# Kernel tuning notes

Measured on AMD Instinct MI355X. Metric: run time of the kernel, lower is better.

Reference implementation:

```python
import jax, jax.numpy as jnp
import numpy as np

C = 1203      # num_classes
P = 0.8       # mitigation exponent
Q = 2.0       # compensation exponent
EPS = 0.01
LOSS_WEIGHT = 1.0


def setup_inputs() -> dict:
    key = jax.random.key(0)
    k1, k2 = jax.random.split(key)
    N = 32768
    cls_score = jax.random.normal(k1, (N, C + 2), dtype=jnp.float32)
    labels = jax.random.randint(k2, (N,), 0, C, dtype=jnp.int64)  # all positive RoIs
    label_weights = jnp.ones((N,), dtype=jnp.float32)
    return {
        'cls_score': cls_score,
        'labels': labels,
        'label_weights': label_weights,
        'avg_factor': N,
    }


def _seesaw_loss(cls_score, labels, label_weights, avg_factor):
    N = cls_score.shape[0]
    rows = jnp.arange(N)

    # cum_samples buffer: starts at zero, incremented by per-class counts this step
    cum = jnp.zeros((C + 1,), cls_score.dtype).at[labels].add(1.0)

    # one-hot multi-labels over C+1 channels (last channel is background, unused since all labels < C)
    m_labels = jax.nn.one_hot(labels, C + 1, dtype=cls_score.dtype)  # [N, C+1]

    csc = cls_score[:, :C]   # class logits [N, C]
    csb = cls_score[:, C:]   # binary (pos/neg) logits [N, 2]

    # --- seesaw weights ---
    cum_c = jnp.maximum(cum, 1.0)
    ratio = cum_c[None, :] / cum_c[:, None]                 # [C+1, C+1]
    sample_w = jnp.where(ratio < 1.0, ratio ** P, 1.0)
    mitigation = sample_w[labels]                           # [N, C+1]

    scores = jax.lax.stop_gradient(jax.nn.softmax(csc, axis=1))  # detached
    self_scores = scores[rows, labels]                      # [N]
    score_mat = scores / jnp.maximum(self_scores, EPS)[:, None]  # [N, C]
    compensation = jnp.where(score_mat > 1.0, score_mat ** Q, 1.0)

    seesaw = mitigation.at[:, :C].multiply(compensation)    # [N, C+1]

    # add log seesaw weights to negative-class logits
    adj = csc + (jnp.log(seesaw) * (1.0 - m_labels))[:, :C]  # [N, C]

    # --- multi-label cross entropy (per-row masked logsumexp + softplus) ---
    lw = label_weights[:, None]
    pos_mask = m_labels[:, :C] * lw            # [N, C]
    neg_mask = (1.0 - m_labels[:, :C]) * lw
    ninf = jnp.array(-jnp.inf, adj.dtype)
    pos_lse = jax.nn.logsumexp(jnp.where(pos_mask == 1.0, -adj, ninf), axis=1)
    neg_lse = jax.nn.logsumexp(jnp.where(neg_mask == 1.0, adj, ninf), axis=1)
    inv_pos_log = -jnp.log(pos_mask.sum(axis=1))
    loss_classes = LOSS_WEIGHT * jax.nn.softplus(inv_pos_log + pos_lse + neg_lse).sum() / avg_factor

    # --- binary objectness cross entropy ---
    b_labels = (labels == C).astype(jnp.int32)  # all zero here
    ce = -jax.nn.log_softmax(csb, axis=1)[rows, b_labels]
    loss_binary = (ce * label_weights).sum() / avg_factor

    return loss_classes + loss_binary


def reference(cls_score, labels, label_weights, avg_factor):
    return _seesaw_loss(cls_score, labels, label_weights, avg_factor)
```

## Files before the change

### kernel.cpp

```cpp
#include <hip/hip_runtime.h>


#define C_CLS   1203
#define ROW_LEN 1205
#define NBINS   1204
#define PADLEN  1280
#define NEG_HUGE (-3.402823466e38f)
#define LOG2E    1.4426950408889634f
#define LN2      0.6931471805599453f
#define LOG_EPS2 (-6.643856189774724f)
#define P_POW    0.8f
#define Q_POW    2.0f
#define M2FIX    16.0f

#if __has_builtin(__builtin_amdgcn_exp2f)
#define EXP2(x) __builtin_amdgcn_exp2f(x)
#else
#define EXP2(x) exp2f(x)
#endif
#if __has_builtin(__builtin_amdgcn_logf)
#define LOG2F_(x) __builtin_amdgcn_logf(x)
#else
#define LOG2F_(x) __log2f(x)
#endif

__launch_bounds__(1024)
__global__ void prep_k(const int* __restrict__ labels, int N,
                       float* __restrict__ plgG) {
    __shared__ unsigned hist[NBINS];
    for (int i = threadIdx.x; i < NBINS; i += 1024) hist[i] = 0u;
    __syncthreads();

    const int nv = N >> 2;
    const int4* lp = (const int4*)labels;
    for (int i = threadIdx.x; i < nv; i += 1024) {
        int4 v = lp[i];
        atomicAdd(&hist[v.x], 1u); atomicAdd(&hist[v.y], 1u);
        atomicAdd(&hist[v.z], 1u); atomicAdd(&hist[v.w], 1u);
    }
    for (int i = (N & ~3) + (int)threadIdx.x; i < N; i += 1024)
        atomicAdd(&hist[labels[i]], 1u);
    __syncthreads();

    for (int u = threadIdx.x; u < PADLEN; u += 1024) {
        float v = 0.0f;
        if (u < NBINS) v = P_POW * LOG2F_(fmaxf((float)hist[u], 1.0f));
        plgG[u] = v;
    }
}

__launch_bounds__(256, 8)
__global__ void seesaw_row_k(const float* __restrict__ cls,
                             const int* __restrict__ labels,
                             const float* __restrict__ lweights,
                             const float* __restrict__ plgG,
                             float* __restrict__ wsums,
                             int N) {
    __shared__ __align__(16) float plg[PADLEN];
    {
        const float4* src = (const float4*)plgG;
        float4* dst = (float4*)plg;
        for (int i = threadIdx.x; i < PADLEN / 4; i += 256) dst[i] = src[i];
    }
    __syncthreads();

    const int lane = threadIdx.x & 63;
    const int wv   = threadIdx.x >> 6;
    const int wid  = blockIdx.x * 4 + wv;
    const int nw   = gridDim.x * 4;

    float acc = 0.0f;
    int n = wid;
    if (n < N) {
        int   labc = labels[n];
        float wc   = lweights[n];
        for (;;) {
            const int  n2    = n + nw;
            const bool have2 = (n2 < N);
            int labn = 0; float wn = 0.0f;
            if (have2) { labn = labels[n2]; wn = lweights[n2]; }

            const float* row = cls + (size_t)n * ROW_LEN;
            const int k = (-n) & 3;
            const float labv = row[labc];
            const float c0   = row[C_CLS];
            const float c1   = row[C_CLS + 1];

            const float4* vp = (const float4*)(row + k);
            float4 q[5];
            #pragma unroll
            for (int i = 0; i < 4; ++i) q[i] = vp[(size_t)i * 64 + lane];
            {
                int b4 = k + 1024 + 4 * lane;
                float4 t = make_float4(NEG_HUGE, NEG_HUGE, NEG_HUGE, NEG_HUGE);
                if (b4 + 3 <= C_CLS - 1) {
                    t = vp[(size_t)256 + lane];
                } else {
                    if (b4     <= C_CLS - 1) t.x = row[b4];
                    if (b4 + 1 <= C_CLS - 1) t.y = row[b4 + 1];
                    if (b4 + 2 <= C_CLS - 1) t.z = row[b4 + 2];
                }
                q[4] = t;
            }
            float pv = (lane < k) ? row[lane] : NEG_HUGE;

            pv *= LOG2E;
            float s = EXP2(pv - M2FIX);
            #pragma unroll
            for (int i = 0; i < 5; ++i) {
                q[i].x *= LOG2E; q[i].y *= LOG2E;
                q[i].z *= LOG2E; q[i].w *= LOG2E;
                s += EXP2(q[i].x - M2FIX) + EXP2(q[i].y - M2FIX)
                   + EXP2(q[i].z - M2FIX) + EXP2(q[i].w - M2FIX);
            }
            #pragma unroll
            for (int o = 32; o > 0; o >>= 1) s += __shfl_xor(s, o, 64);

            const float L2    = M2FIX + LOG2F_(s);
            const float labv2 = labv * LOG2E;
            const float G     = fmaxf(labv2, L2 + LOG_EPS2);
            const float W     = L2 - Q_POW * (G - L2);
            const float plogl = plg[labc];

            float T;
            {
                float t1 = fminf(plg[lane] - plogl, 0.0f);
                float h  = fmaxf(pv - G, 0.0f);
                T = EXP2((pv - W) + fmaf(Q_POW, h, t1));
            }
            #pragma unroll
            for (int i = 0; i < 5; ++i) {
                const int u = k + 256 * i + 4 * lane;
                float lg0 = plg[u], lg1 = plg[u + 1], lg2 = plg[u + 2], lg3 = plg[u + 3];
                { float t1 = fminf(lg0 - plogl, 0.f), h = fmaxf(q[i].x - G, 0.f);
                  T += EXP2((q[i].x - W) + fmaf(Q_POW, h, t1)); }
                { float t1 = fminf(lg1 - plogl, 0.f), h = fmaxf(q[i].y - G, 0.f);
                  T += EXP2((q[i].y - W) + fmaf(Q_POW, h, t1)); }
                { float t1 = fminf(lg2 - plogl, 0.f), h = fmaxf(q[i].z - G, 0.f);
                  T += EXP2((q[i].z - W) + fmaf(Q_POW, h, t1)); }
                { float t1 = fminf(lg3 - plogl, 0.f), h = fmaxf(q[i].w - G, 0.f);
                  T += EXP2((q[i].w - W) + fmaf(Q_POW, h, t1)); }
            }
            #pragma unroll
            for (int o = 32; o > 0; o >>= 1) T += __shfl_xor(T, o, 64);
            T -= EXP2(labv2 - W);
            T = fmaxf(T, 1e-37f);

            const float nl2 = W + LOG2F_(T);
            const float xx  = (nl2 - labv2) * LN2;
            const float rl  = (xx > 0.0f) ? (xx + log1pf(__expf(-xx)))
                                          : log1pf(__expf(xx));
            const float mm   = fmaxf(c0, c1);
            const float lseb = mm + __logf(__expf(c0 - mm) + __expf(c1 - mm));
            const float ce   = lseb - ((labc == C_CLS) ? c1 : c0);
            const float rlw  = (wc == 1.0f) ? rl : 0.0f;
            acc += rlw + ce * wc;

            if (!have2) break;
            n = n2; labc = labn; wc = wn;
        }
    }

    if (lane == 0) wsums[wid] = acc;
}

__launch_bounds__(512)
__global__ void reduce_k(const float* __restrict__ wsums, int nb,
                         const int* __restrict__ avg_raw,
                         float* __restrict__ out) {
    int tid = threadIdx.x;
    float s = 0.0f;
    int nb4 = nb >> 2;
    const float4* bp = (const float4*)wsums;
    for (int i = tid; i < nb4; i += 512) {
        float4 v = bp[i];
        s += (v.x + v.y) + (v.z + v.w);
    }
    for (int i = (nb4 << 2) + tid; i < nb; i += 512) s += wsums[i];

    #pragma unroll
    for (int o = 32; o > 0; o >>= 1) s += __shfl_xor(s, o, 64);

    __shared__ float ws8[8];
    int lane = tid & 63, wvi = tid >> 6;
    if (lane == 0) ws8[wvi] = s;
    __syncthreads();
    if (tid == 0) {
        float t = 0.0f;
        #pragma unroll
        for (int i = 0; i < 8; ++i) t += ws8[i];
        int ai = avg_raw[0];
        float af;
        if (ai > 0 && ai < (1 << 26)) {
            af = (float)ai;
        } else {
            union { int i; float f; } u;
            u.i = ai;
            af = u.f;
        }
        out[0] = t / af;
    }
}

extern "C" void kernel_launch(void* const* d_in, const int* in_sizes, int n_in,
                              void* d_out, int out_size, void* d_ws, size_t ws_size,
                              hipStream_t stream) {
    const float* cls    = (const float*)d_in[0];
    const int*   labels = (const int*)d_in[1];
    const float* lw     = (const float*)d_in[2];
    const int*   avgp   = (const int*)d_in[3];
    float*       out    = (float*)d_out;

    const int N = in_sizes[1];

    float* plgG  = (float*)d_ws;
    float* wsums = (float*)d_ws + PADLEN;

    int g = (N + 15) / 16;
    if (g > 2048) g = 2048;
    if (g < 1) g = 1;

    prep_k<<<1, 1024, 0, stream>>>(labels, N, plgG);
    seesaw_row_k<<<g, 256, 0, stream>>>(cls, labels, lw, plgG, wsums, N);
    reduce_k<<<1, 512, 0, stream>>>(wsums, g * 4, avgp, out);
}
```

Before: 48.61 us.

## Prefetch next row into registers and use pre-shifted LDS tables for float4 reads

New measurement: 169.3 us. 248% more time.

```diff
diff --git a/kernel.cpp b/kernel.cpp
--- a/kernel.cpp
+++ b/kernel.cpp
@@ -4,7 +4,7 @@
 #define C_CLS   1203
 #define ROW_LEN 1205
 #define NBINS   1204
-#define PADLEN  1280
+#define RPAD    1280
 #define NEG_HUGE (-3.402823466e38f)
 #define LOG2E    1.4426950408889634f
 #define LN2      0.6931471805599453f
@@ -42,12 +42,32 @@
         atomicAdd(&hist[labels[i]], 1u);
     __syncthreads();
 
-    for (int u = threadIdx.x; u < PADLEN; u += 1024) {
-        float v = 0.0f;
-        if (u < NBINS) v = P_POW * LOG2F_(fmaxf((float)hist[u], 1.0f));
-        plgG[u] = v;
-    }
-}
+    for (int u = threadIdx.x; u < RPAD; u += 1024) {
+        #pragma unroll
+        for (int kk = 0; kk < 4; ++kk) {
+            int j = u + kk;
+            float v = 0.0f;
+            if (j < NBINS) v = P_POW * LOG2F_(fmaxf((float)hist[j], 1.0f));
+            plgG[kk * RPAD + u] = v;
+        }
+    }
+}
+
+#define LOADV(n_, label_, q_, pv_, labv_, c0_, c1_, k_) do {                    \
+    const float* row_ = cls + (size_t)(n_) * ROW_LEN;                           \
+    labv_ = row_[label_]; c0_ = row_[C_CLS]; c1_ = row_[C_CLS + 1];             \
+    const float4* vp_ = (const float4*)(row_ + (k_));                           \
+    _Pragma("unroll")                                                           \
+    for (int i_ = 0; i_ < 4; ++i_) q_[i_] = vp_[(size_t)i_ * 64 + lane];        \
+    {   int b4_ = (k_) + 1024 + 4 * lane;                                       \
+        float4 t_ = make_float4(NEG_HUGE, NEG_HUGE, NEG_HUGE, NEG_HUGE);        \
+        if (b4_ + 3 <= C_CLS - 1) { t_ = vp_[(size_t)256 + lane]; }             \
+        else { if (b4_     <= C_CLS - 1) t_.x = row_[b4_];                      \
+               if (b4_ + 1 <= C_CLS - 1) t_.y = row_[b4_ + 1];                  \
+               if (b4_ + 2 <= C_CLS - 1) t_.z = row_[b4_ + 2]; }                \
+        q_[4] = t_; }                                                           \
+    pv_ = (lane < (k_)) ? row_[lane] : NEG_HUGE;                                \
+} while (0)
 
 __launch_bounds__(256, 8)
 __global__ void seesaw_row_k(const float* __restrict__ cls,
@@ -56,11 +76,11 @@
                              const float* __restrict__ plgG,
                              float* __restrict__ wsums,
                              int N) {
-    __shared__ __align__(16) float plg[PADLEN];
+    __shared__ __align__(16) float plg[4][RPAD];
     {
         const float4* src = (const float4*)plgG;
-        float4* dst = (float4*)plg;
-        for (int i = threadIdx.x; i < PADLEN / 4; i += 256) dst[i] = src[i];
+        float4* dst = (float4*)&plg[0][0];
+        for (int i = threadIdx.x; i < RPAD; i += 256) dst[i] = src[i];
     }
     __syncthreads();
 
@@ -72,37 +92,20 @@
     float acc = 0.0f;
     int n = wid;
     if (n < N) {
+        const int k = (-n) & 3;
         int   labc = labels[n];
         float wc   = lweights[n];
+        float4 q[5]; float pv, labv, c0, c1;
+        LOADV(n, labc, q, pv, labv, c0, c1, k);
+
         for (;;) {
             const int  n2    = n + nw;
             const bool have2 = (n2 < N);
-            int labn = 0; float wn = 0.0f;
-            if (have2) { labn = labels[n2]; wn = lweights[n2]; }
-
-            const float* row = cls + (size_t)n * ROW_LEN;
-            const int k = (-n) & 3;
-            const float labv = row[labc];
-            const float c0   = row[C_CLS];
-            const float c1   = row[C_CLS + 1];
-
-            const float4* vp = (const float4*)(row + k);
-            float4 q[5];
-            #pragma unroll
-            for (int i = 0; i < 4; ++i) q[i] = vp[(size_t)i * 64 + lane];
-            {
-                int b4 = k + 1024 + 4 * lane;
-                float4 t = make_float4(NEG_HUGE, NEG_HUGE, NEG_HUGE, NEG_HUGE);
-                if (b4 + 3 <= C_CLS - 1) {
-                    t = vp[(size_t)256 + lane];
-                } else {
-                    if (b4     <= C_CLS - 1) t.x = row[b4];
-                    if (b4 + 1 <= C_CLS - 1) t.y = row[b4 + 1];
-                    if (b4 + 2 <= C_CLS - 1) t.z = row[b4 + 2];
-                }
-                q[4] = t;
-            }
-            float pv = (lane < k) ? row[lane] : NEG_HUGE;
+            float4 qn[5]; float pvn, labvn, c0n, c1n; int labn; float wn;
+            if (have2) {
+                labn = labels[n2]; wn = lweights[n2];
+                LOADV(n2, labn, qn, pvn, labvn, c0n, c1n, k);
+            }
 
             pv *= LOG2E;
             float s = EXP2(pv - M2FIX);
@@ -119,27 +122,28 @@
             const float L2    = M2FIX + LOG2F_(s);
             const float labv2 = labv * LOG2E;
             const float G     = fmaxf(labv2, L2 + LOG_EPS2);
-            const float W     = L2 - Q_POW * (G - L2);
-            const float plogl = plg[labc];
+            const float W     = L2 + Q_POW * (L2 - G);
+            const float plogl = plg[0][labc];
+            const float Wp    = W + plogl;
+            const float mW    = -W;
 
             float T;
             {
-                float t1 = fminf(plg[lane] - plogl, 0.0f);
-                float h  = fmaxf(pv - G, 0.0f);
-                T = EXP2((pv - W) + fmaf(Q_POW, h, t1));
+                float t = fminf(plg[0][lane] - Wp, mW);
+                float h = fmaxf(pv - G, 0.0f);
+                T = EXP2(fmaf(Q_POW, h, pv) + t);
             }
             #pragma unroll
             for (int i = 0; i < 5; ++i) {
-                const int u = k + 256 * i + 4 * lane;
-                float lg0 = plg[u], lg1 = plg[u + 1], lg2 = plg[u + 2], lg3 = plg[u + 3];
-                { float t1 = fminf(lg0 - plogl, 0.f), h = fmaxf(q[i].x - G, 0.f);
-                  T += EXP2((q[i].x - W) + fmaf(Q_POW, h, t1)); }
-                { float t1 = fminf(lg1 - plogl, 0.f), h = fmaxf(q[i].y - G, 0.f);
-                  T += EXP2((q[i].y - W) + fmaf(Q_POW, h, t1)); }
-                { float t1 = fminf(lg2 - plogl, 0.f), h = fmaxf(q[i].z - G, 0.f);
-                  T += EXP2((q[i].z - W) + fmaf(Q_POW, h, t1)); }
-                { float t1 = fminf(lg3 - plogl, 0.f), h = fmaxf(q[i].w - G, 0.f);
-                  T += EXP2((q[i].w - W) + fmaf(Q_POW, h, t1)); }
+                const float4 lg = *(const float4*)&plg[k][256 * i + 4 * lane];
+                { float t = fminf(lg.x - Wp, mW), h = fmaxf(q[i].x - G, 0.f);
+                  T += EXP2(fmaf(Q_POW, h, q[i].x) + t); }
+                { float t = fminf(lg.y - Wp, mW), h = fmaxf(q[i].y - G, 0.f);
+                  T += EXP2(fmaf(Q_POW, h, q[i].y) + t); }
+                { float t = fminf(lg.z - Wp, mW), h = fmaxf(q[i].z - G, 0.f);
+                  T += EXP2(fmaf(Q_POW, h, q[i].z) + t); }
+                { float t = fminf(lg.w - Wp, mW), h = fmaxf(q[i].w - G, 0.f);
+                  T += EXP2(fmaf(Q_POW, h, q[i].w) + t); }
             }
             #pragma unroll
             for (int o = 32; o > 0; o >>= 1) T += __shfl_xor(T, o, 64);
@@ -158,6 +162,9 @@
 
             if (!have2) break;
             n = n2; labc = labn; wc = wn;
+            labv = labvn; c0 = c0n; c1 = c1n; pv = pvn;
+            #pragma unroll
+            for (int i = 0; i < 5; ++i) q[i] = qn[i];
         }
     }
 
@@ -214,7 +221,7 @@
     const int N = in_sizes[1];
 
     float* plgG  = (float*)d_ws;
-    float* wsums = (float*)d_ws + PADLEN;
+    float* wsums = (float*)d_ws + 4 * RPAD;
 
     int g = (N + 15) / 16;
     if (g > 2048) g = 2048;
```
